# Kernel tuning notes

Measured on AMD Instinct MI355X. Metric: run time of the kernel, lower is better.

## Reference

```python
import jax, jax.numpy as jnp
import numpy as np

B, S, D, H, E, TOPK = 8, 1024, 512, 2048, 8, 2


def setup_inputs() -> dict:
    key = jax.random.key(0)
    ks = jax.random.split(key, 7)
    scale = 0.02
    return {
        "x": jax.random.normal(ks[0], (B, S, D), jnp.float32),
        "gate_w": jax.random.normal(ks[1], (D, E), jnp.float32) * scale,
        "gate_b": jnp.zeros((E,), jnp.float32),
        "w1": jax.random.normal(ks[2], (E, D, H), jnp.float32) * scale,
        "b1": jnp.zeros((E, H), jnp.float32),
        "w2": jax.random.normal(ks[3], (E, H, D), jnp.float32) * scale,
        "b2": jnp.zeros((E, D), jnp.float32),
    }


def reference(x, gate_w, gate_b, w1, b1, w2, b2):
    # ---- MoE transformer MLP (fastmoe FMoETransformerMLP, NaiveGate) ----
    xt = x.reshape(-1, D)                       # [T, D], T = B*S tokens
    logits = xt @ gate_w + gate_b               # [T, E]
    top_val, top_idx = jax.lax.top_k(logits, TOPK)  # [T, k]
    score = jax.nn.softmax(top_val, axis=-1)    # softmax over the k selected logits

    y = jnp.zeros_like(xt)
    # Loop over the small fixed expert set; each token's combine weight for
    # expert e is the sum of its top-k scores routed to e (0 if not selected).
    for e in range(E):
        w_tok = jnp.sum(score * (top_idx == e), axis=-1)        # [T]
        h = jax.nn.gelu(xt @ w1[e] + b1[e], approximate=False)  # [T, H]
        y = y + w_tok[:, None] * (h @ w2[e] + b2[e])            # [T, D]

    y = y.reshape(B, S, D)
    # Outer model: log_softmax over seq of channel-summed features
    return jax.nn.log_softmax(jnp.sum(y, axis=2), axis=1)       # [B, S]
```

## Files before the change

### kernel.cpp

```cpp
#include <hip/hip_runtime.h>
#include <hip/hip_bf16.h>
#include <math.h>

#define T_TOK 8192
#define DIM   512
#define NEXP  8
#define HID   2048
#define NBAT  8
#define SEQ   1024

typedef short  short8 __attribute__((ext_vector_type(8)));
typedef float  f32x4  __attribute__((ext_vector_type(4)));

__device__ __forceinline__ unsigned short f2bf(float f) {
    union { float f; unsigned int u; } v; v.f = f;
    unsigned int u = v.u;
    unsigned int r = u + 0x7FFFu + ((u >> 16) & 1u);
    return (unsigned short)(r >> 16);
}

__device__ __forceinline__ float gelu_f(float v) {
    float v2 = v * v;
    float w = v * (-2.302344f - 0.102955f * v2);
    return v / (1.f + __builtin_amdgcn_exp2f(w));
}

__global__ void prep_gate_k(const float* __restrict__ w1, unsigned short* __restrict__ w1f,
                            const float* __restrict__ w2, const float* __restrict__ b2,
                            float* __restrict__ w2sum, float* __restrict__ b2sum,
                            int* __restrict__ counts,
                            const float* __restrict__ x, const float* __restrict__ gw,
                            const float* __restrict__ gb,
                            unsigned short* __restrict__ xb,
                            int* __restrict__ eidx, float* __restrict__ esc0,
                            float* __restrict__ esc1) {
    int bid = blockIdx.x;
    int tid = threadIdx.x;
    int wave = tid >> 6, lane = tid & 63;
    if (bid < 2048) {
        __shared__ unsigned short tile[64][68];
        int e = bid >> 8, r = bid & 255;
        int d0 = (r & 7) * 64, h0 = (r >> 3) * 64;
        const float* src = w1 + (size_t)e * DIM * HID;
        #pragma unroll
        for (int pass = 0; pass < 4; ++pass) {
            int dr = pass * 16 + (tid >> 4);
            int hc = (tid & 15) * 4;
            float4 v = *(const float4*)(src + (size_t)(d0 + dr) * HID + h0 + hc);
            tile[hc + 0][dr] = f2bf(v.x);
            tile[hc + 1][dr] = f2bf(v.y);
            tile[hc + 2][dr] = f2bf(v.z);
            tile[hc + 3][dr] = f2bf(v.w);
        }
        __syncthreads();
        int l = tid & 63, q = l >> 4, c = l & 15;
        int kk0 = (r & 7) * 2, g0 = (r >> 3) * 4;
        #pragma unroll
        for (int pi = 0; pi < 2; ++pi) {
            int sub = pi * 4 + wave;
            int kk2 = sub >> 2, g2 = sub & 3;
            const unsigned short* tp = &tile[g2 * 16 + c][kk2 * 32 + q * 8];
            ushort4 a = *(const ushort4*)(tp);
            ushort4 b = *(const ushort4*)(tp + 4);
            unsigned short* dst = w1f +
                ((size_t)(e * 128 + g0 + g2) * 16 + kk0 + kk2) * 512 + l * 8;
            *(ushort4*)(dst)     = a;
            *(ushort4*)(dst + 4) = b;
        }
    } else if (bid < 4096) {
        int t = (bid - 2048) * 4 + wave;
        const float* xp = x + (size_t)t * DIM;
        unsigned short* xbp = xb + (size_t)t * DIM;
        float acc[8] = {0, 0, 0, 0, 0, 0, 0, 0};
        #pragma unroll
        for (int it = 0; it < 8; ++it) {
            int d = it * 64 + lane;
            float xv = xp[d];
            xbp[d] = f2bf(xv);
            float4 g0 = *(const float4*)(gw + d * 8);
            float4 g1 = *(const float4*)(gw + d * 8 + 4);
            acc[0] += xv * g0.x; acc[1] += xv * g0.y; acc[2] += xv * g0.z; acc[3] += xv * g0.w;
            acc[4] += xv * g1.x; acc[5] += xv * g1.y; acc[6] += xv * g1.z; acc[7] += xv * g1.w;
        }
        #pragma unroll
        for (int e = 0; e < 8; ++e) {
            float s = acc[e];
            #pragma unroll
            for (int off = 32; off >= 1; off >>= 1) s += __shfl_xor(s, off);
            acc[e] = s + gb[e];
        }
        float v0 = -1e30f, v1 = -1e30f; int i0 = 0, i1 = 0;
        #pragma unroll
        for (int e = 0; e < 8; ++e) {
            float v = acc[e];
            if (v > v0) { v1 = v0; i1 = i0; v0 = v; i0 = e; }
            else if (v > v1) { v1 = v; i1 = e; }
        }
        float e1 = expf(v1 - v0);
        float inv = 1.f / (1.f + e1);
        if (lane == 0) {
            eidx[t] = i0 | (i1 << 4);
            esc0[t] = inv;
            esc1[t] = e1 * inv;
        }
    } else if (bid < 8192) {
        int row = (bid - 4096) * 4 + wave;
        const float* p = w2 + (size_t)row * DIM;
        float4 a = *(const float4*)(p + lane * 4);
        float4 b = *(const float4*)(p + 256 + lane * 4);
        float s = a.x + a.y + a.z + a.w + b.x + b.y + b.z + b.w;
        #pragma unroll
        for (int off = 32; off >= 1; off >>= 1) s += __shfl_xor(s, off);
        if (lane == 0) w2sum[row] = s;
    } else {
        if (tid < 8) counts[tid] = 0;
        for (int r = wave; r < NEXP; r += 4) {
            const float* p = b2 + (size_t)r * DIM;
            float s = 0.f;
            for (int i = lane; i < DIM; i += 64) s += p[i];
            #pragma unroll
            for (int off = 32; off >= 1; off >>= 1) s += __shfl_xor(s, off);
            if (lane == 0) b2sum[r] = s;
        }
    }
}

__global__ __launch_bounds__(1024) void route_k(
    const int* __restrict__ eidx, const float* __restrict__ esc0,
    const float* __restrict__ esc1, const float* __restrict__ b2sum,
    int* __restrict__ counts,
    int* __restrict__ ptok, float* __restrict__ pscore,
    float* __restrict__ s_partial) {
    int tid = threadIdx.x;
    int t = blockIdx.x * 1024 + tid;
    int wv = tid >> 6, lane = tid & 63;
    int pk = eidx[t];
    int i0 = pk & 0xf, i1 = (pk >> 4) & 0xf;
    float s0 = esc0[t], s1 = esc1[t];

    s_partial[t] = s0 * b2sum[i0] + s1 * b2sum[i1];

    __shared__ int waveCnt[16][8];
    __shared__ int waveBase[16][8];

    unsigned long long m0[8], m1[8];
    #pragma unroll
    for (int e = 0; e < 8; ++e) {
        m0[e] = __ballot(i0 == e);
        m1[e] = __ballot(i1 == e);
    }
    if (lane < 8) {
        int c = 0;
        #pragma unroll
        for (int e = 0; e < 8; ++e)
            if (lane == e) c = __popcll(m0[e]) + __popcll(m1[e]);
        waveCnt[wv][lane] = c;
    }
    __syncthreads();
    if (tid < 8) {
        int e = tid;
        int total = 0;
        #pragma unroll
        for (int w = 0; w < 16; ++w) total += waveCnt[w][e];
        int base = atomicAdd(&counts[e], total);
        int run = base;
        #pragma unroll
        for (int w = 0; w < 16; ++w) {
            waveBase[w][e] = run;
            run += waveCnt[w][e];
        }
    }
    __syncthreads();

    unsigned long long lt = (1ULL << lane) - 1ULL;
    int slot0 = 0, slot1 = 0;
    #pragma unroll
    for (int e = 0; e < 8; ++e) {
        if (i0 == e) slot0 = waveBase[wv][e] + __popcll(m0[e] & lt);
        if (i1 == e) slot1 = waveBase[wv][e] + __popcll(m0[e]) + __popcll(m1[e] & lt);
    }
    ptok[i0 * T_TOK + slot0] = t;  pscore[i0 * T_TOK + slot0] = s0;
    ptok[i1 * T_TOK + slot1] = t;  pscore[i1 * T_TOK + slot1] = s1;
}

#define GPTR(p) (const __attribute__((address_space(1))) void*)(p)
#define LPTR(p) (__attribute__((address_space(3))) void*)(p)

__global__ __launch_bounds__(256, 3) void moe_gemm_k(
    const unsigned short* __restrict__ xb, const unsigned short* __restrict__ w1f,
    const float* __restrict__ b1, const float* __restrict__ w2sum,
    const int* __restrict__ counts, const int* __restrict__ ptok,
    const float* __restrict__ pscore, float* __restrict__ s_partial) {

    int flat = blockIdx.x + (int)blockIdx.y * 135;
    int xcd = flat & 7;
    int s = flat >> 3;
    int bx = s >> 1;
    int hBase = (xcd * 2 + (s & 1)) * 128;

    int e = 8, rowBase = 0, accT = 0;
    #pragma unroll
    for (int i = 0; i < 8; ++i) {
        int nt = (counts[i] + 127) >> 7;
        if (e == 8 && bx < accT + nt) { e = i; rowBase = (bx - accT) * 128; }
        accT += nt;
    }
    if (e == 8) return;
    int n_e = counts[e];

    __shared__ unsigned short A_s[2][128 * 64];
    __shared__ int   tokLds[128];
    __shared__ float scoreLds[128];

    int tid = threadIdx.x;
    int wave = tid >> 6, lane = tid & 63;

    if (tid < 128) {
        int r = rowBase + tid;
        bool valid = r < n_e;
        tokLds[tid]   = valid ? ptok[e * T_TOK + r]   : 0;
        scoreLds[tid] = valid ? pscore[e * T_TOK + r] : 0.f;
    }
    __syncthreads();

    unsigned gAo[4];
    #pragma unroll
    for (int i = 0; i < 4; ++i) {
        int c = i * 256 + tid;
        int row = c >> 3, pos = c & 7;
        int j = (pos ^ (row & 7)) * 8;
        gAo[i] = (unsigned)tokLds[row] * DIM + j;
    }

    int wm = wave >> 1, wn = wave & 1;
    int quad = lane >> 4, col = lane & 15;

    f32x4 acc[4][4];
    #pragma unroll
    for (int m = 0; m < 4; ++m)
        #pragma unroll
        for (int n = 0; n < 4; ++n)
            acc[m][n] = (f32x4){0.f, 0.f, 0.f, 0.f};

    int aOff0 = (wm * 64 + col) * 64 + ((((0 << 2) | quad) ^ (col & 7)) * 8);
    int aOff1 = (wm * 64 + col) * 64 + ((((1 << 2) | quad) ^ (col & 7)) * 8);

    const unsigned short* bp = w1f +
        (size_t)(e * 128 + (hBase >> 4) + wn * 4) * 8192 + lane * 8;
    short8 bf0[4], bf1[4];

    #pragma unroll
    for (int i = 0; i < 4; ++i)
        __builtin_amdgcn_global_load_lds(GPTR(xb + gAo[i]), LPTR(&A_s[0][i * 2048 + tid * 8]), 16, 0, 0);
    __builtin_amdgcn_sched_barrier(0);
    #pragma unroll
    for (int i = 0; i < 4; ++i)
        __builtin_amdgcn_global_load_lds(GPTR(xb + gAo[i] + 64), LPTR(&A_s[1][i * 2048 + tid * 8]), 16, 0, 0);
    __builtin_amdgcn_sched_barrier(0);
    #pragma unroll
    for (int n = 0; n < 4; ++n) bf0[n] = *(const short8*)(bp + n * 8192);
    __builtin_amdgcn_sched_barrier(0);

    #pragma unroll
    for (int kk = 0; kk < 8; ++kk) {
        const int cur = kk & 1;
        if (kk == 0)      { asm volatile("s_waitcnt vmcnt(8)"  ::: "memory"); }
        else if (kk == 7) { asm volatile("s_waitcnt vmcnt(12)" ::: "memory"); }
        else              { asm volatile("s_waitcnt vmcnt(16)" ::: "memory"); }
        __builtin_amdgcn_s_barrier();

        #pragma unroll
        for (int n = 0; n < 4; ++n)
            bf1[n] = *(const short8*)(bp + (2 * kk + 1) * 512 + n * 8192);

        short8 af0[4], af1[4];
        const unsigned short* aB = &A_s[cur][0];
        #pragma unroll
        for (int m = 0; m < 4; ++m) af0[m] = *(const short8*)(aB + aOff0 + m * 1024);
        #pragma unroll
        for (int m = 0; m < 4; ++m) af1[m] = *(const short8*)(aB + aOff1 + m * 1024);
        asm volatile("s_waitcnt lgkmcnt(0)" ::: "memory");
        __builtin_amdgcn_s_barrier();

        if (kk < 6) {
            int ko = (kk + 2) * 64;
            #pragma unroll
            for (int i = 0; i < 4; ++i)
                __builtin_amdgcn_global_load_lds(GPTR(xb + gAo[i] + ko), LPTR(&A_s[cur][i * 2048 + tid * 8]), 16, 0, 0);
        }
        __builtin_amdgcn_sched_barrier(0);

        __builtin_amdgcn_s_setprio(1);
        #pragma unroll
        for (int m = 0; m < 4; ++m)
            #pragma unroll
            for (int n = 0; n < 4; ++n)
                acc[m][n] = __builtin_amdgcn_mfma_f32_16x16x32_bf16(af0[m], bf0[n], acc[m][n], 0, 0, 0);
        __builtin_amdgcn_s_setprio(0);

        if (kk < 7) {
            #pragma unroll
            for (int n = 0; n < 4; ++n)
                bf0[n] = *(const short8*)(bp + (2 * kk + 2) * 512 + n * 8192);
        }
        __builtin_amdgcn_sched_barrier(0);

        __builtin_amdgcn_s_setprio(1);
        #pragma unroll
        for (int m = 0; m < 4; ++m)
            #pragma unroll
            for (int n = 0; n < 4; ++n)
                acc[m][n] = __builtin_amdgcn_mfma_f32_16x16x32_bf16(af1[m], bf1[n], acc[m][n], 0, 0, 0);
        __builtin_amdgcn_s_setprio(0);
    }

    const float* b1e = b1 + e * HID;
    const float* w2e = w2sum + e * HID;
    float bias[4], wsum[4];
    #pragma unroll
    for (int n = 0; n < 4; ++n) {
        int h = hBase + wn * 64 + n * 16 + col;
        bias[n] = b1e[h];
        wsum[n] = w2e[h];
    }
    #pragma unroll
    for (int m = 0; m < 4; ++m) {
        float rp0 = 0.f, rp1 = 0.f, rp2 = 0.f, rp3 = 0.f;
        #pragma unroll
        for (int n = 0; n < 4; ++n) {
            rp0 += gelu_f(acc[m][n][0] + bias[n]) * wsum[n];
            rp1 += gelu_f(acc[m][n][1] + bias[n]) * wsum[n];
            rp2 += gelu_f(acc[m][n][2] + bias[n]) * wsum[n];
            rp3 += gelu_f(acc[m][n][3] + bias[n]) * wsum[n];
        }
        #pragma unroll
        for (int off = 8; off >= 1; off >>= 1) {
            rp0 += __shfl_xor(rp0, off);
            rp1 += __shfl_xor(rp1, off);
            rp2 += __shfl_xor(rp2, off);
            rp3 += __shfl_xor(rp3, off);
        }
        if (col < 4) {
            float mine = (col == 0) ? rp0 : (col == 1) ? rp1 : (col == 2) ? rp2 : rp3;
            int rl = wm * 64 + m * 16 + quad * 4 + col;
            int r = rowBase + rl;
            if (r < n_e)
                atomicAdd(&s_partial[tokLds[rl]], scoreLds[rl] * mine);
        }
    }
}

__global__ void lsm_k(const float* __restrict__ s, float* __restrict__ out) {
    int b = blockIdx.x, tid = threadIdx.x;
    int wave = tid >> 6, lane = tid & 63;
    __shared__ float red[4];
    const float* sp = s + (size_t)b * SEQ;
    float v[4];
    #pragma unroll
    for (int i = 0; i < 4; ++i) v[i] = sp[tid + i * 256];
    float m = fmaxf(fmaxf(v[0], v[1]), fmaxf(v[2], v[3]));
    #pragma unroll
    for (int off = 32; off >= 1; off >>= 1) m = fmaxf(m, __shfl_xor(m, off));
    if (lane == 0) red[wave] = m;
    __syncthreads();
    m = fmaxf(fmaxf(red[0], red[1]), fmaxf(red[2], red[3]));
    __syncthreads();
    float t = 0.f;
    #pragma unroll
    for (int i = 0; i < 4; ++i) t += expf(v[i] - m);
    #pragma unroll
    for (int off = 32; off >= 1; off >>= 1) t += __shfl_xor(t, off);
    if (lane == 0) red[wave] = t;
    __syncthreads();
    t = red[0] + red[1] + red[2] + red[3];
    float L = m + logf(t);
    #pragma unroll
    for (int i = 0; i < 4; ++i) out[(size_t)b * SEQ + tid + i * 256] = v[i] - L;
}

extern "C" void kernel_launch(void* const* d_in, const int* in_sizes, int n_in,
                              void* d_out, int out_size, void* d_ws, size_t ws_size,
                              hipStream_t stream) {
    const float* x  = (const float*)d_in[0];
    const float* gw = (const float*)d_in[1];
    const float* gb = (const float*)d_in[2];
    const float* w1 = (const float*)d_in[3];
    const float* b1 = (const float*)d_in[4];
    const float* w2 = (const float*)d_in[5];
    const float* b2 = (const float*)d_in[6];
    float* out = (float*)d_out;

    char* ws = (char*)d_ws;
    int*   counts    = (int*)  (ws + 0);
    float* b2sum     = (float*)(ws + 1280);
    float* s_partial = (float*)(ws + 1536);
    float* w2sum     = (float*)(ws + 34304);
    int*   ptok      = (int*)  (ws + 99840);
    float* pscore    = (float*)(ws + 361984);
    int*   eidx      = (int*)  (ws + 624128);
    float* esc0      = (float*)(ws + 656896);
    float* esc1      = (float*)(ws + 689664);
    unsigned short* xb  = (unsigned short*)(ws + 722432);
    unsigned short* w1f = (unsigned short*)(ws + 9111040);

    prep_gate_k<<<8193, 256, 0, stream>>>(w1, w1f, w2, b2, w2sum, b2sum, counts,
                                          x, gw, gb, xb, eidx, esc0, esc1);
    route_k<<<NEXP, 1024, 0, stream>>>(eidx, esc0, esc1, b2sum, counts, ptok, pscore, s_partial);
    moe_gemm_k<<<dim3(135, 16), 256, 0, stream>>>(xb, w1f, b1, w2sum, counts, ptok, pscore, s_partial);
    lsm_k<<<NBAT, 256, 0, stream>>>(s_partial, out);
}
```

Before: 182.0 us.

## Fuse token routing into gate kernel via per-token atomics, fold bias seed into log-softmax

Removes the separate route_k launch. Each token's gate wave now claims its expert slots with global atomicAdd on counts and writes ptok/pscore directly. The b2sum seed term is moved from the routing step into lsm_k, and s_partial is zeroed in the gate kernel. counts is zeroed with a memset before the launch, which trades one kernel launch for a memset node plus 16K contended global atomics on 8 counters. Slot order per expert becomes nondeterministic, which may hurt row locality in the GEMM gather.

```diff
diff --git a/kernel.cpp b/kernel.cpp
--- a/kernel.cpp
+++ b/kernel.cpp
@@ -33,7 +33,9 @@
                             const float* __restrict__ gb,
                             unsigned short* __restrict__ xb,
                             int* __restrict__ eidx, float* __restrict__ esc0,
-                            float* __restrict__ esc1) {
+                            float* __restrict__ esc1,
+                            int* __restrict__ ptok, float* __restrict__ pscore,
+                            float* __restrict__ s_partial) {
     int bid = blockIdx.x;
     int tid = threadIdx.x;
     int wave = tid >> 6, lane = tid & 63;
@@ -98,10 +100,16 @@
         }
         float e1 = expf(v1 - v0);
         float inv = 1.f / (1.f + e1);
+        float s0 = inv, s1 = e1 * inv;
         if (lane == 0) {
             eidx[t] = i0 | (i1 << 4);
-            esc0[t] = inv;
-            esc1[t] = e1 * inv;
+            esc0[t] = s0;
+            esc1[t] = s1;
+            s_partial[t] = 0.f;
+            int slot0 = atomicAdd(&counts[i0], 1);
+            int slot1 = atomicAdd(&counts[i1], 1);
+            ptok[i0 * T_TOK + slot0] = t;  pscore[i0 * T_TOK + slot0] = s0;
+            ptok[i1 * T_TOK + slot1] = t;  pscore[i1 * T_TOK + slot1] = s1;
         }
     } else if (bid < 8192) {
         int row = (bid - 4096) * 4 + wave;
@@ -113,7 +121,6 @@
         for (int off = 32; off >= 1; off >>= 1) s += __shfl_xor(s, off);
         if (lane == 0) w2sum[row] = s;
     } else {
-        if (tid < 8) counts[tid] = 0;
         for (int r = wave; r < NEXP; r += 4) {
             const float* p = b2 + (size_t)r * DIM;
             float s = 0.f;
@@ -123,64 +130,6 @@
             if (lane == 0) b2sum[r] = s;
         }
     }
-}
-
-__global__ __launch_bounds__(1024) void route_k(
-    const int* __restrict__ eidx, const float* __restrict__ esc0,
-    const float* __restrict__ esc1, const float* __restrict__ b2sum,
-    int* __restrict__ counts,
-    int* __restrict__ ptok, float* __restrict__ pscore,
-    float* __restrict__ s_partial) {
-    int tid = threadIdx.x;
-    int t = blockIdx.x * 1024 + tid;
-    int wv = tid >> 6, lane = tid & 63;
-    int pk = eidx[t];
-    int i0 = pk & 0xf, i1 = (pk >> 4) & 0xf;
-    float s0 = esc0[t], s1 = esc1[t];
-
-    s_partial[t] = s0 * b2sum[i0] + s1 * b2sum[i1];
-
-    __shared__ int waveCnt[16][8];
-    __shared__ int waveBase[16][8];
-
-    unsigned long long m0[8], m1[8];
-    #pragma unroll
-    for (int e = 0; e < 8; ++e) {
-        m0[e] = __ballot(i0 == e);
-        m1[e] = __ballot(i1 == e);
-    }
-    if (lane < 8) {
-        int c = 0;
-        #pragma unroll
-        for (int e = 0; e < 8; ++e)
-            if (lane == e) c = __popcll(m0[e]) + __popcll(m1[e]);
-        waveCnt[wv][lane] = c;
-    }
-    __syncthreads();
-    if (tid < 8) {
-        int e = tid;
-        int total = 0;
-        #pragma unroll
-        for (int w = 0; w < 16; ++w) total += waveCnt[w][e];
-        int base = atomicAdd(&counts[e], total);
-        int run = base;
-        #pragma unroll
-        for (int w = 0; w < 16; ++w) {
-            waveBase[w][e] = run;
-            run += waveCnt[w][e];
-        }
-    }
-    __syncthreads();
-
-    unsigned long long lt = (1ULL << lane) - 1ULL;
-    int slot0 = 0, slot1 = 0;
-    #pragma unroll
-    for (int e = 0; e < 8; ++e) {
-        if (i0 == e) slot0 = waveBase[wv][e] + __popcll(m0[e] & lt);
-        if (i1 == e) slot1 = waveBase[wv][e] + __popcll(m0[e]) + __popcll(m1[e] & lt);
-    }
-    ptok[i0 * T_TOK + slot0] = t;  pscore[i0 * T_TOK + slot0] = s0;
-    ptok[i1 * T_TOK + slot1] = t;  pscore[i1 * T_TOK + slot1] = s1;
 }
 
 #define GPTR(p) (const __attribute__((address_space(1))) void*)(p)
@@ -350,14 +299,21 @@
     }
 }
 
-__global__ void lsm_k(const float* __restrict__ s, float* __restrict__ out) {
+__global__ void lsm_k(const float* __restrict__ s, const int* __restrict__ eidx,
+                      const float* __restrict__ esc0, const float* __restrict__ esc1,
+                      const float* __restrict__ b2sum, float* __restrict__ out) {
     int b = blockIdx.x, tid = threadIdx.x;
     int wave = tid >> 6, lane = tid & 63;
     __shared__ float red[4];
     const float* sp = s + (size_t)b * SEQ;
     float v[4];
     #pragma unroll
-    for (int i = 0; i < 4; ++i) v[i] = sp[tid + i * 256];
+    for (int i = 0; i < 4; ++i) {
+        int t = b * SEQ + tid + i * 256;
+        int pk = eidx[t];
+        float seed = esc0[t] * b2sum[pk & 0xf] + esc1[t] * b2sum[(pk >> 4) & 0xf];
+        v[i] = sp[tid + i * 256] + seed;
+    }
     float m = fmaxf(fmaxf(v[0], v[1]), fmaxf(v[2], v[3]));
     #pragma unroll
     for (int off = 32; off >= 1; off >>= 1) m = fmaxf(m, __shfl_xor(m, off));
@@ -403,9 +359,10 @@
     unsigned short* xb  = (unsigned short*)(ws + 722432);
     unsigned short* w1f = (unsigned short*)(ws + 9111040);
 
+    hipMemsetAsync(counts, 0, NEXP * sizeof(int), stream);
     prep_gate_k<<<8193, 256, 0, stream>>>(w1, w1f, w2, b2, w2sum, b2sum, counts,
-                                          x, gw, gb, xb, eidx, esc0, esc1);
-    route_k<<<NEXP, 1024, 0, stream>>>(eidx, esc0, esc1, b2sum, counts, ptok, pscore, s_partial);
+                                          x, gw, gb, xb, eidx, esc0, esc1,
+                                          ptok, pscore, s_partial);
     moe_gemm_k<<<dim3(135, 16), 256, 0, stream>>>(xb, w1f, b1, w2sum, counts, ptok, pscore, s_partial);
-    lsm_k<<<NBAT, 256, 0, stream>>>(s_partial, out);
-}
+    lsm_k<<<NBAT, 256, 0, stream>>>(s_partial, eidx, esc0, esc1, b2sum, out);
+}
```

Measured after the change: 360.6 us. 98.1% more time.
